# Optimization experiments

Hardware: AMD Instinct MI355X
Metric: run time of the kernel (lower is better)

The kernel has to match this reference:

```python
import jax, jax.numpy as jnp
import numpy as np

EMBED_DIM = 256
N_HEADS = 16
DK = EMBED_DIM // N_HEADS


def setup_inputs() -> dict:
    key = jax.random.key(0)
    ks = jax.random.split(key, 7)
    B, N, D = 32, 10000, EMBED_DIM
    scale = 1.0 / np.sqrt(D)
    ctx = jax.random.normal(ks[0], (B, D), dtype=jnp.float32)
    node_emb = jax.random.normal(ks[1], (B, N, D), dtype=jnp.float32)
    feas_mask = jax.random.randint(ks[2], (B, N), 0, 2).astype(jnp.bool_)
    Wq = jax.random.normal(ks[3], (D, D), dtype=jnp.float32) * scale
    Wk = jax.random.normal(ks[4], (D, D), dtype=jnp.float32) * scale
    Wv = jax.random.normal(ks[5], (D, D), dtype=jnp.float32) * scale
    Wo = jax.random.normal(ks[6], (D, D), dtype=jnp.float32) * scale
    return {"ctx": ctx, "node_emb": node_emb, "feas_mask": feas_mask,
            "Wq": Wq, "Wk": Wk, "Wv": Wv, "Wo": Wo}


def reference(ctx, node_emb, feas_mask, Wq, Wk, Wv, Wo):
    B, N, D = node_emb.shape
    H, dk = N_HEADS, DK
    # torch nn.Linear(no bias): y = x @ W.T
    q = (ctx @ Wq.T).reshape(B, H, dk)                    # [B,H,dk]
    k = (node_emb @ Wk.T).reshape(B, N, H, dk)            # [B,N,H,dk]
    v = (node_emb @ Wv.T).reshape(B, N, H, dk)            # [B,N,H,dk]
    logits = jnp.einsum('bhd,bnhd->bhn', q, k) / jnp.sqrt(jnp.float32(dk))
    neg_inf = jnp.finfo(logits.dtype).min
    logits = jnp.where(feas_mask[:, None, :], logits, neg_inf)
    attn = jax.nn.softmax(logits, axis=-1)                # [B,H,N]
    head_ctx = jnp.einsum('bhn,bnhd->bhd', attn, v)       # [B,H,dk]
    out = head_ctx.reshape(B, D)
    return out @ Wo.T
```

## Files before the change

### kernel.cpp

```cpp
#include <hip/hip_runtime.h>
#include <math.h>

#define NB 32
#define NN 10000
#define DIM 256
#define NH 16
#define NPART 32
#define PREC2 4112
#define IDXSTRIDE 10240

typedef short short8v __attribute__((ext_vector_type(8)));
typedef float float4v __attribute__((ext_vector_type(4)));

__device__ __forceinline__ unsigned bf16rne(float f) {
    unsigned u = __float_as_uint(f);
    return (u + 0x7FFFu + ((u >> 16) & 1u)) >> 16;
}
__device__ __forceinline__ unsigned pack2(float a, float b) {
    return bf16rne(a) | (bf16rne(b) << 16);
}
__device__ __forceinline__ short8v pack8(float4 A, float4 B) {
    union { short8v s; unsigned u[4]; } r;
    r.u[0] = pack2(A.x, A.y); r.u[1] = pack2(A.z, A.w);
    r.u[2] = pack2(B.x, B.y); r.u[3] = pack2(B.z, B.w);
    return r.s;
}
#define SWB(d) ((((d) >> 1) & 7) << 4)

__global__ void prep_compact_kernel(const float* __restrict__ ctx,
                                    const float* __restrict__ Wq,
                                    const float* __restrict__ Wk,
                                    const void* __restrict__ maskp,
                                    float* __restrict__ wt,
                                    int* __restrict__ idx,
                                    int* __restrict__ cnt) {
    int bid = blockIdx.x;
    int t = threadIdx.x, lane = t & 63, w = t >> 6;

    __shared__ float ctxL[DIM];
    __shared__ float qL[64];
    __shared__ int sflag;
    __shared__ int wcnt[4];

    if (bid < 4 * NB) {
        int b = bid >> 2, iq = bid & 3;
        ctxL[t] = ctx[b * DIM + t];
        __syncthreads();

        float4 c = ((const float4*)ctxL)[lane];
        for (int i = iq * 64 + w; i < iq * 64 + 64; i += 4) {
            float4 wq = ((const float4*)(Wq + (size_t)i * DIM))[lane];
            float s = wq.x * c.x + wq.y * c.y + wq.z * c.z + wq.w * c.w;
            #pragma unroll
            for (int off = 1; off < 64; off <<= 1) s += __shfl_xor(s, off, 64);
            if (lane == 0) qL[i - iq * 64] = s;
        }
        __syncthreads();

        #pragma unroll
        for (int hh = 0; hh < 4; ++hh) {
            int h = iq * 4 + hh;
            float a = 0.f;
            #pragma unroll
            for (int j = 0; j < 16; ++j)
                a += qL[hh * 16 + j] * Wk[(size_t)(h * 16 + j) * DIM + t];
            wt[((size_t)b * NH + h) * DIM + t] = 0.25f * a;
        }
    } else {
        int b = bid - 4 * NB;
        const int* wordbase = (const int*)maskp + (size_t)b * (NN / 4);
        int bad = 0;
        for (int i = t; i < NN / 4; i += 256)
            if ((unsigned)wordbase[i] > 1u) bad = 1;
        if (t == 0) sflag = 0;
        __syncthreads();
        if (bad) sflag = 1;
        __syncthreads();
        const bool bytemask = (sflag != 0);
        const unsigned char* m8 = (const unsigned char*)maskp + (size_t)b * NN;
        const int* m32 = (const int*)maskp + (size_t)b * NN;

        int segbeg = w * (NN / 4);
        int segend = segbeg + (NN / 4);

        int c1 = 0;
        for (int base = segbeg; base < segend; base += 64) {
            int i = base + lane;
            int pred = (i < segend) ? (bytemask ? (m8[i] != 0) : (m32[i] != 0)) : 0;
            unsigned long long bal = __ballot(pred);
            c1 += __popcll(bal);
        }
        if (lane == 0) wcnt[w] = c1;
        __syncthreads();

        int run = 0;
        for (int k = 0; k < w; ++k) run += wcnt[k];

        int* ob = idx + (size_t)b * IDXSTRIDE;
        for (int base = segbeg; base < segend; base += 64) {
            int i = base + lane;
            int pred = (i < segend) ? (bytemask ? (m8[i] != 0) : (m32[i] != 0)) : 0;
            unsigned long long bal = __ballot(pred);
            int rank = __popcll(bal & ((1ull << lane) - 1ull));
            if (pred) ob[run + rank] = i;
            run += __popcll(bal);
        }
        if (t == 0) cnt[b] = wcnt[0] + wcnt[1] + wcnt[2] + wcnt[3];
    }
}

__launch_bounds__(256, 4)
__global__ void attend_kernel(const float* __restrict__ node,
                              const int* __restrict__ idx,
                              const int* __restrict__ cntarr,
                              const float* __restrict__ wt,
                              float* __restrict__ partials) {
    __shared__ __align__(16) char smem[35328];
    char* XT = smem;
    char* PL = smem + 32768;
    float* LL = (float*)(smem + 35072);

    int b = blockIdx.x / NPART;
    int part = blockIdx.x % NPART;
    int t = threadIdx.x, lane = t & 63;
    int w = __builtin_amdgcn_readfirstlane(t >> 6);
    int hq = lane & 15, g = lane >> 4;

    int cnt = cntarr[b];
    int psz = ((cnt + NPART * 64 - 1) / (NPART * 64)) * 64;
    int n0 = part * psz;
    int n1 = n0 + psz; if (n1 > cnt) n1 = cnt;

    const float* nb = node + (size_t)b * NN * DIM;
    const int* ib = idx + (size_t)b * IDXSTRIDE;

    short8v wfrag0, wfrag1, wfrag2, wfrag3, wfrag4, wfrag5, wfrag6, wfrag7;
    {
        const float* wrow = wt + ((size_t)b * NH + hq) * DIM + g * 8;
        #define WLOAD(cc) wfrag##cc = pack8(*(const float4*)(wrow + cc * 32), \
                                            *(const float4*)(wrow + cc * 32 + 4));
        WLOAD(0) WLOAD(1) WLOAD(2) WLOAD(3) WLOAD(4) WLOAD(5) WLOAD(6) WLOAD(7)
        #undef WLOAD
    }

    float4v accB0 = (float4v){0.f,0.f,0.f,0.f};
    float4v accB1 = accB0, accB2 = accB0, accB3 = accB0;
    float lacc = 0.f;
    int ln2 = (16 * w + hq) * 2;

    for (int tb = n0; tb < n1; tb += 64) {
        __syncthreads();

        float4v acc = (float4v){0.f, 0.f, 0.f, 0.f};
        {
            int pos = tb + 16 * w + hq;
            if (pos > cnt - 1) pos = cnt - 1;
            int ni = ib[pos];
            const float* arow = nb + (size_t)ni * DIM + g * 8;
            #define STEP_A(cc) { \
                float4 A = *(const float4*)(arow + cc * 32); \
                float4 B = *(const float4*)(arow + cc * 32 + 4); \
                short8v af = pack8(A, B); \
                union { short8v s; unsigned short u[8]; } U; U.s = af; \
                int d0 = g * 8 + cc * 32; \
                _Pragma("unroll") \
                for (int j = 0; j < 8; ++j) \
                    *(unsigned short*)(XT + (size_t)(d0 + j) * 128 + \
                                       (ln2 ^ SWB(d0 + j))) = U.u[j]; \
                acc = __builtin_amdgcn_mfma_f32_16x16x32_bf16(af, wfrag##cc, acc, 0, 0, 0); \
            }
            STEP_A(0) STEP_A(1) STEP_A(2) STEP_A(3)
            STEP_A(4) STEP_A(5) STEP_A(6) STEP_A(7)
            #undef STEP_A
        }

        int mb_ = tb + 16 * w + 4 * g;
        float p0 = (mb_ + 0 < n1) ? __expf(acc[0]) : 0.f;
        float p1 = (mb_ + 1 < n1) ? __expf(acc[1]) : 0.f;
        float p2 = (mb_ + 2 < n1) ? __expf(acc[2]) : 0.f;
        float p3 = (mb_ + 3 < n1) ? __expf(acc[3]) : 0.f;
        float ts = p0 + p1 + p2 + p3;
        ts += __shfl_xor(ts, 16, 64);
        ts += __shfl_xor(ts, 32, 64);
        lacc += ts;
        *(uint2*)(PL + hq * 144 + (16 * w + 4 * g) * 2) =
            make_uint2(pack2(p0, p1), pack2(p2, p3));

        __syncthreads();

        #pragma unroll
        for (int chunk = 0; chunk < 2; ++chunk) {
            short8v pf = *(const short8v*)(PL + hq * 144 + chunk * 64 + g * 16);
            int d0 = 64 * w + hq;
            short8v xf0 = *(const short8v*)(XT + (size_t)(d0) * 128 +
                                            ((chunk * 64 + g * 16) ^ SWB(d0)));
            short8v xf1 = *(const short8v*)(XT + (size_t)(d0 + 16) * 128 +
                                            ((chunk * 64 + g * 16) ^ SWB(d0 + 16)));
            short8v xf2 = *(const short8v*)(XT + (size_t)(d0 + 32) * 128 +
                                            ((chunk * 64 + g * 16) ^ SWB(d0 + 32)));
            short8v xf3 = *(const short8v*)(XT + (size_t)(d0 + 48) * 128 +
                                            ((chunk * 64 + g * 16) ^ SWB(d0 + 48)));
            accB0 = __builtin_amdgcn_mfma_f32_16x16x32_bf16(xf0, pf, accB0, 0, 0, 0);
            accB1 = __builtin_amdgcn_mfma_f32_16x16x32_bf16(xf1, pf, accB1, 0, 0, 0);
            accB2 = __builtin_amdgcn_mfma_f32_16x16x32_bf16(xf2, pf, accB2, 0, 0, 0);
            accB3 = __builtin_amdgcn_mfma_f32_16x16x32_bf16(xf3, pf, accB3, 0, 0, 0);
        }
    }

    __syncthreads();
    float* GL = (float*)smem;
    #pragma unroll
    for (int r = 0; r < 4; ++r) {
        GL[hq * 260 + 64 * w +  0 + 4 * g + r] = accB0[r];
        GL[hq * 260 + 64 * w + 16 + 4 * g + r] = accB1[r];
        GL[hq * 260 + 64 * w + 32 + 4 * g + r] = accB2[r];
        GL[hq * 260 + 64 * w + 48 + 4 * g + r] = accB3[r];
    }
    if (lane < 16) LL[w * 16 + lane] = lacc;
    __syncthreads();

    float* rec = partials + (size_t)blockIdx.x * PREC2;
    if (t < NH) rec[t] = LL[t] + LL[16 + t] + LL[32 + t] + LL[48 + t];
    for (int i = t; i < NH * DIM; i += 256)
        rec[16 + i] = GL[(i >> 8) * 260 + (i & 255)];
}

__global__ void reduce_hc_kernel(const float* __restrict__ partials,
                                 const float* __restrict__ Wv,
                                 float* __restrict__ hcws) {
    int b = blockIdx.x >> 4, h = blockIdx.x & 15;
    int t = threadIdx.x;
    __shared__ float grow[DIM];
    __shared__ float lp[NPART];
    __shared__ float lsum;

    const float* pb = partials + (size_t)b * NPART * PREC2;
    float a = 0.f;
    for (int p = 0; p < NPART; ++p) a += pb[(size_t)p * PREC2 + 16 + h * DIM + t];
    grow[t] = a;
    if (t < NPART) lp[t] = pb[(size_t)t * PREC2 + h];
    __syncthreads();
    if (t == 0) {
        float s = 0.f;
        #pragma unroll
        for (int p = 0; p < NPART; ++p) s += lp[p];
        lsum = s;
    }
    __syncthreads();

    int i = h * 16 + (t >> 4), sub = t & 15;
    const float4* wrow = (const float4*)(Wv + (size_t)i * DIM + sub * 16);
    const float4* gr = (const float4*)(grow + sub * 16);
    float s = 0.f;
    #pragma unroll
    for (int k = 0; k < 4; ++k) {
        float4 wv = wrow[k], gv = gr[k];
        s += wv.x * gv.x + wv.y * gv.y + wv.z * gv.z + wv.w * gv.w;
    }
    s += __shfl_xor(s, 1, 64);
    s += __shfl_xor(s, 2, 64);
    s += __shfl_xor(s, 4, 64);
    s += __shfl_xor(s, 8, 64);
    if (sub == 0) hcws[(size_t)b * DIM + i] = s / lsum;
}

__global__ void out_kernel(const float* __restrict__ hcws,
                           const float* __restrict__ Wo,
                           float* __restrict__ out) {
    int b = blockIdx.x >> 3, o = blockIdx.x & 7;
    int t = threadIdx.x;
    int e = o * 32 + (t >> 3), sub = t & 7;
    const float4* wrow = (const float4*)(Wo + (size_t)e * DIM + sub * 32);
    const float4* hrow = (const float4*)(hcws + (size_t)b * DIM + sub * 32);
    float a = 0.f;
    #pragma unroll
    for (int k = 0; k < 8; ++k) {
        float4 wv = wrow[k], hv = hrow[k];
        a += wv.x * hv.x + wv.y * hv.y + wv.z * hv.z + wv.w * hv.w;
    }
    a += __shfl_xor(a, 1, 64);
    a += __shfl_xor(a, 2, 64);
    a += __shfl_xor(a, 4, 64);
    if (sub == 0) out[(size_t)b * DIM + e] = a;
}

extern "C" void kernel_launch(void* const* d_in, const int* in_sizes, int n_in,
                              void* d_out, int out_size, void* d_ws, size_t ws_size,
                              hipStream_t stream) {
    const float* ctx  = (const float*)d_in[0];
    const float* node = (const float*)d_in[1];
    const void*  mask = (const void*)d_in[2];
    const float* Wq   = (const float*)d_in[3];
    const float* Wk   = (const float*)d_in[4];
    const float* Wv   = (const float*)d_in[5];
    const float* Wo   = (const float*)d_in[6];
    float* out = (float*)d_out;

    float* wsf = (float*)d_ws;
    float* wt = wsf;
    float* hcws = wt + (size_t)NB * NH * DIM;
    int*   cnt = (int*)(hcws + (size_t)NB * DIM);
    int*   idx = cnt + 256;
    float* partials = (float*)(idx + (size_t)NB * IDXSTRIDE);

    prep_compact_kernel<<<NB * 4 + NB, 256, 0, stream>>>(ctx, Wq, Wk, mask, wt, idx, cnt);
    attend_kernel<<<NB * NPART, 256, 0, stream>>>(node, idx, cnt, wt, partials);
    reduce_hc_kernel<<<NB * 16, 256, 0, stream>>>(partials, Wv, hcws);
    out_kernel<<<NB * 8, 256, 0, stream>>>(hcws, Wo, out);
}
```

Measured before the change: 78.55 us.

## Double-buffer attend tiles and overlap phase B with next tile loads

Restructures the attend loop into a software pipeline with double-buffered XT/PL shared-memory tiles. Each iteration issues the global loads and next index fetch for the upcoming tile first, then runs the P·X MFMA phase on the previous buffer, then the logits phase on the current one. This removes one barrier per tile and hides gather latency behind MFMA work. In exchange it doubles shared memory to about 70KB, lowers the occupancy bound to 2 blocks per CU, and halves NPART so each block processes longer segments, which means fewer blocks and fewer partials to reduce.

New measurement: 72.34 us. -7.9%, faster.

```diff
diff --git a/kernel.cpp b/kernel.cpp
--- a/kernel.cpp
+++ b/kernel.cpp
@@ -5,7 +5,7 @@
 #define NN 10000
 #define DIM 256
 #define NH 16
-#define NPART 32
+#define NPART 16
 #define PREC2 4112
 #define IDXSTRIDE 10240
 
@@ -109,16 +109,80 @@
     }
 }
 
-__launch_bounds__(256, 4)
+#define XTBUF(bb) (smem + (size_t)(bb) * 32768)
+#define PLBUF(bb) (smem + 65536 + (size_t)(bb) * 2304)
+
+#define STEP_A(cc) { \
+    short8v af = pack8(LA##cc, LB##cc); \
+    union { short8v s; unsigned short u[8]; } U; U.s = af; \
+    int d0 = g * 8 + cc * 32; \
+    _Pragma("unroll") \
+    for (int j = 0; j < 8; ++j) \
+        *(unsigned short*)(XTc + (size_t)(d0 + j) * 128 + \
+                           (ln2 ^ SWB(d0 + j))) = U.u[j]; \
+    acc = __builtin_amdgcn_mfma_f32_16x16x32_bf16(af, wfrag##cc, acc, 0, 0, 0); \
+}
+
+#define PHASE_A_TAIL(tb_, cur_) { \
+    char* XTc = XTBUF(cur_); char* PLc = PLBUF(cur_); \
+    float4v acc = (float4v){0.f, 0.f, 0.f, 0.f}; \
+    STEP_A(0) STEP_A(1) STEP_A(2) STEP_A(3) \
+    STEP_A(4) STEP_A(5) STEP_A(6) STEP_A(7) \
+    int mb_ = (tb_) + 16 * w + 4 * g; \
+    float p0 = (mb_ + 0 < n1) ? __expf(acc[0]) : 0.f; \
+    float p1 = (mb_ + 1 < n1) ? __expf(acc[1]) : 0.f; \
+    float p2 = (mb_ + 2 < n1) ? __expf(acc[2]) : 0.f; \
+    float p3 = (mb_ + 3 < n1) ? __expf(acc[3]) : 0.f; \
+    float ts = p0 + p1 + p2 + p3; \
+    ts += __shfl_xor(ts, 16, 64); \
+    ts += __shfl_xor(ts, 32, 64); \
+    lacc += ts; \
+    *(uint2*)(PLc + hq * 144 + (16 * w + 4 * g) * 2) = \
+        make_uint2(pack2(p0, p1), pack2(p2, p3)); \
+}
+
+#define PHASE_B(bb) { \
+    char* XTp = XTBUF(bb); char* PLp = PLBUF(bb); \
+    _Pragma("unroll") \
+    for (int chunk = 0; chunk < 2; ++chunk) { \
+        short8v pf = *(const short8v*)(PLp + hq * 144 + chunk * 64 + g * 16); \
+        int d0 = 64 * w + hq; \
+        short8v xf0 = *(const short8v*)(XTp + (size_t)(d0) * 128 + \
+                                        ((chunk * 64 + g * 16) ^ SWB(d0))); \
+        short8v xf1 = *(const short8v*)(XTp + (size_t)(d0 + 16) * 128 + \
+                                        ((chunk * 64 + g * 16) ^ SWB(d0 + 16))); \
+        short8v xf2 = *(const short8v*)(XTp + (size_t)(d0 + 32) * 128 + \
+                                        ((chunk * 64 + g * 16) ^ SWB(d0 + 32))); \
+        short8v xf3 = *(const short8v*)(XTp + (size_t)(d0 + 48) * 128 + \
+                                        ((chunk * 64 + g * 16) ^ SWB(d0 + 48))); \
+        accB0 = __builtin_amdgcn_mfma_f32_16x16x32_bf16(xf0, pf, accB0, 0, 0, 0); \
+        accB1 = __builtin_amdgcn_mfma_f32_16x16x32_bf16(xf1, pf, accB1, 0, 0, 0); \
+        accB2 = __builtin_amdgcn_mfma_f32_16x16x32_bf16(xf2, pf, accB2, 0, 0, 0); \
+        accB3 = __builtin_amdgcn_mfma_f32_16x16x32_bf16(xf3, pf, accB3, 0, 0, 0); \
+    } \
+}
+
+#define LOAD_TILE(nextpos_) \
+    const float* arow = nb + (size_t)ni * DIM + g * 8; \
+    float4 LA0 = *(const float4*)(arow + 0),   LB0 = *(const float4*)(arow + 4); \
+    float4 LA1 = *(const float4*)(arow + 32),  LB1 = *(const float4*)(arow + 36); \
+    float4 LA2 = *(const float4*)(arow + 64),  LB2 = *(const float4*)(arow + 68); \
+    float4 LA3 = *(const float4*)(arow + 96),  LB3 = *(const float4*)(arow + 100); \
+    float4 LA4 = *(const float4*)(arow + 128), LB4 = *(const float4*)(arow + 132); \
+    float4 LA5 = *(const float4*)(arow + 160), LB5 = *(const float4*)(arow + 164); \
+    float4 LA6 = *(const float4*)(arow + 192), LB6 = *(const float4*)(arow + 196); \
+    float4 LA7 = *(const float4*)(arow + 224), LB7 = *(const float4*)(arow + 228); \
+    int ni_next = ib[nextpos_]; \
+    __builtin_amdgcn_sched_group_barrier(0x20, 17, 0);
+
+__launch_bounds__(256, 2)
 __global__ void attend_kernel(const float* __restrict__ node,
                               const int* __restrict__ idx,
                               const int* __restrict__ cntarr,
                               const float* __restrict__ wt,
                               float* __restrict__ partials) {
-    __shared__ __align__(16) char smem[35328];
-    char* XT = smem;
-    char* PL = smem + 32768;
-    float* LL = (float*)(smem + 35072);
+    __shared__ __align__(16) char smem[70400];
+    float* LL = (float*)(smem + 70144);
 
     int b = blockIdx.x / NPART;
     int part = blockIdx.x % NPART;
@@ -147,64 +211,36 @@
     float4v accB1 = accB0, accB2 = accB0, accB3 = accB0;
     float lacc = 0.f;
     int ln2 = (16 * w + hq) * 2;
-
-    for (int tb = n0; tb < n1; tb += 64) {
-        __syncthreads();
-
-        float4v acc = (float4v){0.f, 0.f, 0.f, 0.f};
+    int lastk = 0;
+
+    if (n0 < n1) {
+        int pos = n0 + 16 * w + hq; if (pos > cnt - 1) pos = cnt - 1;
+        int ni = ib[pos];
         {
-            int pos = tb + 16 * w + hq;
-            if (pos > cnt - 1) pos = cnt - 1;
-            int ni = ib[pos];
-            const float* arow = nb + (size_t)ni * DIM + g * 8;
-            #define STEP_A(cc) { \
-                float4 A = *(const float4*)(arow + cc * 32); \
-                float4 B = *(const float4*)(arow + cc * 32 + 4); \
-                short8v af = pack8(A, B); \
-                union { short8v s; unsigned short u[8]; } U; U.s = af; \
-                int d0 = g * 8 + cc * 32; \
-                _Pragma("unroll") \
-                for (int j = 0; j < 8; ++j) \
-                    *(unsigned short*)(XT + (size_t)(d0 + j) * 128 + \
-                                       (ln2 ^ SWB(d0 + j))) = U.u[j]; \
-                acc = __builtin_amdgcn_mfma_f32_16x16x32_bf16(af, wfrag##cc, acc, 0, 0, 0); \
-            }
-            STEP_A(0) STEP_A(1) STEP_A(2) STEP_A(3)
-            STEP_A(4) STEP_A(5) STEP_A(6) STEP_A(7)
-            #undef STEP_A
-        }
-
-        int mb_ = tb + 16 * w + 4 * g;
-        float p0 = (mb_ + 0 < n1) ? __expf(acc[0]) : 0.f;
-        float p1 = (mb_ + 1 < n1) ? __expf(acc[1]) : 0.f;
-        float p2 = (mb_ + 2 < n1) ? __expf(acc[2]) : 0.f;
-        float p3 = (mb_ + 3 < n1) ? __expf(acc[3]) : 0.f;
-        float ts = p0 + p1 + p2 + p3;
-        ts += __shfl_xor(ts, 16, 64);
-        ts += __shfl_xor(ts, 32, 64);
-        lacc += ts;
-        *(uint2*)(PL + hq * 144 + (16 * w + 4 * g) * 2) =
-            make_uint2(pack2(p0, p1), pack2(p2, p3));
-
-        __syncthreads();
-
-        #pragma unroll
-        for (int chunk = 0; chunk < 2; ++chunk) {
-            short8v pf = *(const short8v*)(PL + hq * 144 + chunk * 64 + g * 16);
-            int d0 = 64 * w + hq;
-            short8v xf0 = *(const short8v*)(XT + (size_t)(d0) * 128 +
-                                            ((chunk * 64 + g * 16) ^ SWB(d0)));
-            short8v xf1 = *(const short8v*)(XT + (size_t)(d0 + 16) * 128 +
-                                            ((chunk * 64 + g * 16) ^ SWB(d0 + 16)));
-            short8v xf2 = *(const short8v*)(XT + (size_t)(d0 + 32) * 128 +
-                                            ((chunk * 64 + g * 16) ^ SWB(d0 + 32)));
-            short8v xf3 = *(const short8v*)(XT + (size_t)(d0 + 48) * 128 +
-                                            ((chunk * 64 + g * 16) ^ SWB(d0 + 48)));
-            accB0 = __builtin_amdgcn_mfma_f32_16x16x32_bf16(xf0, pf, accB0, 0, 0, 0);
-            accB1 = __builtin_amdgcn_mfma_f32_16x16x32_bf16(xf1, pf, accB1, 0, 0, 0);
-            accB2 = __builtin_amdgcn_mfma_f32_16x16x32_bf16(xf2, pf, accB2, 0, 0, 0);
-            accB3 = __builtin_amdgcn_mfma_f32_16x16x32_bf16(xf3, pf, accB3, 0, 0, 0);
-        }
+            int posn = n0 + 64 + 16 * w + hq;
+            if (posn > cnt - 1) posn = cnt - 1;
+            LOAD_TILE(posn)
+            PHASE_A_TAIL(n0, 0)
+            ni = ni_next;
+        }
+        __syncthreads();
+
+        for (int tb = n0 + 64; tb < n1; tb += 64) {
+            int k = (tb - n0) >> 6;
+            int cur = k & 1;
+            int posn = tb + 64 + 16 * w + hq;
+            if (posn > cnt - 1) posn = cnt - 1;
+            LOAD_TILE(posn)
+
+            PHASE_B(cur ^ 1)
+            PHASE_A_TAIL(tb, cur)
+
+            ni = ni_next;
+            lastk = k;
+            __syncthreads();
+        }
+
+        PHASE_B(lastk & 1)
     }
 
     __syncthreads();
```
